# Kernel tuning notes

Measured on AMD Instinct MI355X. Metric: run time of the kernel, lower is better.

Reference implementation:

```python
import jax, jax.numpy as jnp
import numpy as np

CHANNELS = 256
BATCH, H, W = 32, 56, 56
K = 26  # round(256 * 0.1)
BOOST_STRENGTH = 1.0


def setup_inputs() -> dict:
    key = jax.random.key(0)
    k1, k2 = jax.random.split(key)
    x = jax.random.normal(k1, (BATCH, CHANNELS, H, W), dtype=jnp.float32)
    duty_cycle = jax.random.uniform(k2, (1, CHANNELS, 1, 1), dtype=jnp.float32)
    return {"x": x, "duty_cycle": duty_cycle, "k": K,
            "boost_strength": jnp.float32(BOOST_STRENGTH)}


def reference(x, duty_cycle, k, boost_strength):
    # boost_activations: x.detach() * exp(-boost_strength * duty_cycle)
    # (boost_strength > 0 in this configuration)
    boosted = jax.lax.stop_gradient(x) * jnp.exp(-boost_strength * duty_cycle)
    # local kwinners: per (b,h,w) location, kthvalue over channels at index
    # C - k + 1 (1-based ascending) == k-th largest boosted value.
    C = x.shape[1]
    sorted_b = jnp.sort(boosted, axis=1)           # ascending over channels
    threshold = sorted_b[:, C - k:C - k + 1, :, :]  # [B,1,H,W], k-th largest
    # off_mask = boosted < threshold; masked_fill with 0 keeps boosted >= threshold
    keep = boosted >= threshold
    return jnp.where(keep, x, jnp.zeros((), dtype=x.dtype))
```

## Files before the change

### kernel.cpp

```cpp
#include <hip/hip_runtime.h>
#include <math.h>

#define C_CH 256
#define KTOP 26
#define HWSZ 3136
#define NPIX 100352
#define CHW  (C_CH * HWSZ)
#define PIX_PER_BLK 32
#define BLKS_PER_IMG 98
#define CPT 32

typedef float f32x4 __attribute__((ext_vector_type(4)));

__device__ __forceinline__ void ce_desc(float& a, float& b) {
    float mx = fmaxf(a, b); float mn = fminf(a, b); a = mx; b = mn;
}
__device__ __forceinline__ void ce_asc(float& a, float& b) {
    float mn = fminf(a, b); float mx = fmaxf(a, b); a = mn; b = mx;
}

__device__ __forceinline__ void sort32_desc(float* v) {
#pragma unroll
    for (int k = 2; k <= 32; k <<= 1) {
#pragma unroll
        for (int j = k >> 1; j > 0; j >>= 1) {
#pragma unroll
            for (int i = 0; i < 32; ++i) {
                int l = i ^ j;
                if (l > i) {
                    if ((i & k) == 0) ce_desc(v[i], v[l]);
                    else              ce_asc(v[i], v[l]);
                }
            }
        }
    }
}

__device__ __forceinline__ void clean32_desc(float* v) {
#pragma unroll
    for (int j = 16; j > 0; j >>= 1) {
#pragma unroll
        for (int i = 0; i < 32; ++i) {
            int l = i ^ j;
            if (l > i) ce_desc(v[i], v[l]);
        }
    }
}

__device__ __forceinline__ void merge26(float* a, const float* __restrict__ src) {
    float h[32];
#pragma unroll
    for (int i = 0; i < 32; ++i) {
        float u = (i < KTOP)      ? a[i]        : -INFINITY;
        float w = (31 - i < KTOP) ? src[31 - i] : -INFINITY;
        h[i] = fmaxf(u, w);
    }
    clean32_desc(h);
#pragma unroll
    for (int j = 0; j < KTOP; ++j) a[j] = h[j];
}

__global__ __launch_bounds__(256, 4) void kwinners_kernel(
    const float* __restrict__ x, const float* __restrict__ duty,
    const float* __restrict__ bsp, float* __restrict__ out)
{
    __shared__ float s[C_CH];
    __shared__ float tile[C_CH][PIX_PER_BLK];
    __shared__ float pub[2][PIX_PER_BLK][26];

    const int t   = threadIdx.x;
    const int w   = t >> 6;
    const int l   = t & 63;
    const int pl  = l & 31;
    const int hf  = l >> 5;
    const int blk = blockIdx.x;
    const int b   = blk / BLKS_PER_IMG;
    const int hw0 = (blk - b * BLKS_PER_IMG) * PIX_PER_BLK;

    {
        const int row0 = w * 64;
        const float* gp = x + (size_t)b * CHW + (size_t)(row0 + (l >> 3)) * HWSZ
                            + hw0 + (l & 7) * 4;
#pragma unroll
        for (int it = 0; it < 8; ++it) {
            __builtin_amdgcn_global_load_lds(
                (const __attribute__((address_space(1))) void*)(gp + (size_t)it * 8 * HWSZ),
                (__attribute__((address_space(3))) void*)&tile[row0 + it * 8][0],
                16, 0, 0);
        }
    }

    {
        float bs = bsp[0];
        float m = -(bs * duty[t]);
        s[t] = (float)exp((double)m);
    }
    __syncthreads();

    const int c0 = w * 64 + hf * 32;
    const float* sc = s + c0;

    float v[CPT];
#pragma unroll
    for (int i = 0; i < CPT; ++i) v[i] = tile[c0 + i][pl] * sc[i];

    sort32_desc(v);

    float a[KTOP];
    {
        float h[32];
#pragma unroll
        for (int i = 0; i < 32; ++i) {
            float u  = (i < KTOP)      ? v[i] : -INFINITY;
            float pw = (31 - i < KTOP) ? __shfl_xor(v[31 - i], 32) : -INFINITY;
            h[i] = fmaxf(u, pw);
        }
        clean32_desc(h);
#pragma unroll
        for (int j = 0; j < KTOP; ++j) a[j] = h[j];
    }

    if ((w & 1) && l < 32) {
        float* dst = pub[w >> 1][pl];
#pragma unroll
        for (int j = 0; j < KTOP; ++j) dst[j] = a[j];
    }
    __syncthreads();

    if (w == 0) {
        merge26(a, pub[0][pl]);
    } else if (w == 2) {
        merge26(a, pub[1][pl]);
        if (l < 32) {
            float* dst = pub[1][pl];
#pragma unroll
            for (int j = 0; j < KTOP; ++j) dst[j] = a[j];
        }
    }
    __syncthreads();

    if (w == 0) {
        const float* src = pub[1][pl];
        float h[32];
#pragma unroll
        for (int i = 0; i < 32; ++i) {
            float u  = (i < KTOP)      ? a[i]        : -INFINITY;
            float wv = (31 - i < KTOP) ? src[31 - i] : -INFINITY;
            h[i] = fmaxf(u, wv);
        }
        float l16[16];
#pragma unroll
        for (int i = 0; i < 16; ++i) l16[i] = fminf(h[i], h[i + 16]);
        float l8[8];
#pragma unroll
        for (int i = 0; i < 8; ++i)  l8[i]  = fminf(l16[i], l16[i + 8]);
        float h4[4];
#pragma unroll
        for (int i = 0; i < 4; ++i)  h4[i]  = fmaxf(l8[i], l8[i + 4]);
        float h2[2];
#pragma unroll
        for (int i = 0; i < 2; ++i)  h2[i]  = fmaxf(h4[i], h4[i + 2]);
        if (l < 32) pub[0][pl][0] = fminf(h2[0], h2[1]);
    }
    __syncthreads();

    {
        const int pg   = l & 7;
        const int r8   = l >> 3;
        const int row0 = w * 64;
        const float t0 = pub[0][pg * 4 + 0][0];
        const float t1 = pub[0][pg * 4 + 1][0];
        const float t2 = pub[0][pg * 4 + 2][0];
        const float t3 = pub[0][pg * 4 + 3][0];

        float* opb = out + (size_t)b * CHW + (size_t)(row0 + r8) * HWSZ
                         + hw0 + pg * 4;
#pragma unroll
        for (int it = 0; it < 8; ++it) {
            const int r = row0 + it * 8 + r8;
            const f32x4 xv = *reinterpret_cast<const f32x4*>(&tile[r][pg * 4]);
            const float scv = s[r];
            f32x4 res;
            res.x = (xv.x * scv >= t0) ? xv.x : 0.0f;
            res.y = (xv.y * scv >= t1) ? xv.y : 0.0f;
            res.z = (xv.z * scv >= t2) ? xv.z : 0.0f;
            res.w = (xv.w * scv >= t3) ? xv.w : 0.0f;
            __builtin_nontemporal_store(
                res, reinterpret_cast<f32x4*>(&opb[(size_t)(it * 8) * HWSZ]));
        }
    }
}

extern "C" void kernel_launch(void* const* d_in, const int* in_sizes, int n_in,
                              void* d_out, int out_size, void* d_ws, size_t ws_size,
                              hipStream_t stream) {
    const float* x    = (const float*)d_in[0];
    const float* duty = (const float*)d_in[1];
    const float* bs   = (const float*)d_in[3];
    float* out = (float*)d_out;

    hipLaunchKernelGGL(kwinners_kernel, dim3(NPIX / PIX_PER_BLK), dim3(256), 0,
                       stream, x, duty, bs, out);
}
```

Measured before the change: 38.39 us.

## Reorganize top-k merge into in-wave shuffles with XOR-swizzled LDS tile

Remaps threads so each wave owns 8 pixels, with 8 lanes each sorting 32 channels of a pixel. The cross-wave merge tree through shared memory and its extra barriers is replaced by in-wave shuffle merges (xor 32, 8, 16). The global-to-LDS tile load and the output store use an XOR swizzle on the pixel-quad column, and the scale array is padded, both to avoid LDS bank conflicts under the new column-strided access. All 64 lanes now do sort and merge work instead of waves idling during the reduction, at the cost of more shuffle traffic and more complex indexing.

```diff
diff --git a/kernel.cpp b/kernel.cpp
--- a/kernel.cpp
+++ b/kernel.cpp
@@ -8,7 +8,6 @@
 #define CHW  (C_CH * HWSZ)
 #define PIX_PER_BLK 32
 #define BLKS_PER_IMG 98
-#define CPT 32
 
 typedef float f32x4 __attribute__((ext_vector_type(4)));
 
@@ -47,12 +46,12 @@
     }
 }
 
-__device__ __forceinline__ void merge26(float* a, const float* __restrict__ src) {
+__device__ __forceinline__ void shfl_merge26(float* a, int mask) {
     float h[32];
 #pragma unroll
     for (int i = 0; i < 32; ++i) {
-        float u = (i < KTOP)      ? a[i]        : -INFINITY;
-        float w = (31 - i < KTOP) ? src[31 - i] : -INFINITY;
+        float u = (i < KTOP)      ? a[i] : -INFINITY;
+        float w = (31 - i < KTOP) ? __shfl_xor(a[31 - i], mask) : -INFINITY;
         h[i] = fmaxf(u, w);
     }
     clean32_desc(h);
@@ -64,28 +63,30 @@
     const float* __restrict__ x, const float* __restrict__ duty,
     const float* __restrict__ bsp, float* __restrict__ out)
 {
-    __shared__ float s[C_CH];
+    __shared__ float s[264];
     __shared__ float tile[C_CH][PIX_PER_BLK];
-    __shared__ float pub[2][PIX_PER_BLK][26];
+    __shared__ float thr_s[PIX_PER_BLK];
 
     const int t   = threadIdx.x;
     const int w   = t >> 6;
     const int l   = t & 63;
-    const int pl  = l & 31;
-    const int hf  = l >> 5;
+    const int g   = l >> 3;
+    const int p3  = l & 7;
+    const int px  = w * 8 + p3;
     const int blk = blockIdx.x;
     const int b   = blk / BLKS_PER_IMG;
     const int hw0 = (blk - b * BLKS_PER_IMG) * PIX_PER_BLK;
 
     {
-        const int row0 = w * 64;
-        const float* gp = x + (size_t)b * CHW + (size_t)(row0 + (l >> 3)) * HWSZ
-                            + hw0 + (l & 7) * 4;
 #pragma unroll
         for (int it = 0; it < 8; ++it) {
+            const int row = w * 64 + it * 8 + g;
+            const int lq  = p3 ^ ((row >> 5) & 7);
+            const float* gp = x + (size_t)b * CHW + (size_t)row * HWSZ
+                                + hw0 + lq * 4;
             __builtin_amdgcn_global_load_lds(
-                (const __attribute__((address_space(1))) void*)(gp + (size_t)it * 8 * HWSZ),
-                (__attribute__((address_space(3))) void*)&tile[row0 + it * 8][0],
+                (const __attribute__((address_space(1))) void*)gp,
+                (__attribute__((address_space(3))) void*)&tile[w * 64 + it * 8][0],
                 16, 0, 0);
         }
     }
@@ -93,16 +94,15 @@
     {
         float bs = bsp[0];
         float m = -(bs * duty[t]);
-        s[t] = (float)exp((double)m);
+        s[(t >> 5) * 33 + (t & 31)] = (float)exp((double)m);
     }
     __syncthreads();
 
-    const int c0 = w * 64 + hf * 32;
-    const float* sc = s + c0;
-
-    float v[CPT];
+    const int pcol = px ^ (g << 2);
+    float v[32];
 #pragma unroll
-    for (int i = 0; i < CPT; ++i) v[i] = tile[c0 + i][pl] * sc[i];
+    for (int i = 0; i < 32; ++i)
+        v[i] = tile[g * 32 + i][pcol] * s[g * 33 + i];
 
     sort32_desc(v);
 
@@ -110,43 +110,23 @@
     {
         float h[32];
 #pragma unroll
-        for (int i = 0; i < 32; ++i) {
-            float u  = (i < KTOP)      ? v[i] : -INFINITY;
-            float pw = (31 - i < KTOP) ? __shfl_xor(v[31 - i], 32) : -INFINITY;
-            h[i] = fmaxf(u, pw);
-        }
+        for (int i = 0; i < 32; ++i)
+            h[i] = fmaxf(v[i], __shfl_xor(v[31 - i], 32));
         clean32_desc(h);
 #pragma unroll
         for (int j = 0; j < KTOP; ++j) a[j] = h[j];
     }
 
-    if ((w & 1) && l < 32) {
-        float* dst = pub[w >> 1][pl];
-#pragma unroll
-        for (int j = 0; j < KTOP; ++j) dst[j] = a[j];
-    }
-    __syncthreads();
+    shfl_merge26(a, 8);
 
-    if (w == 0) {
-        merge26(a, pub[0][pl]);
-    } else if (w == 2) {
-        merge26(a, pub[1][pl]);
-        if (l < 32) {
-            float* dst = pub[1][pl];
-#pragma unroll
-            for (int j = 0; j < KTOP; ++j) dst[j] = a[j];
-        }
-    }
-    __syncthreads();
-
-    if (w == 0) {
-        const float* src = pub[1][pl];
+    float thr;
+    {
         float h[32];
 #pragma unroll
         for (int i = 0; i < 32; ++i) {
-            float u  = (i < KTOP)      ? a[i]        : -INFINITY;
-            float wv = (31 - i < KTOP) ? src[31 - i] : -INFINITY;
-            h[i] = fmaxf(u, wv);
+            float u  = (i < KTOP)      ? a[i] : -INFINITY;
+            float pw = (31 - i < KTOP) ? __shfl_xor(a[31 - i], 16) : -INFINITY;
+            h[i] = fmaxf(u, pw);
         }
         float l16[16];
 #pragma unroll
@@ -160,33 +140,32 @@
         float h2[2];
 #pragma unroll
         for (int i = 0; i < 2; ++i)  h2[i]  = fmaxf(h4[i], h4[i + 2]);
-        if (l < 32) pub[0][pl][0] = fminf(h2[0], h2[1]);
+        thr = fminf(h2[0], h2[1]);
     }
+    if (g == 0) thr_s[px] = thr;
     __syncthreads();
 
     {
-        const int pg   = l & 7;
-        const int r8   = l >> 3;
-        const int row0 = w * 64;
-        const float t0 = pub[0][pg * 4 + 0][0];
-        const float t1 = pub[0][pg * 4 + 1][0];
-        const float t2 = pub[0][pg * 4 + 2][0];
-        const float t3 = pub[0][pg * 4 + 3][0];
-
-        float* opb = out + (size_t)b * CHW + (size_t)(row0 + r8) * HWSZ
-                         + hw0 + pg * 4;
+        const int pg = p3;
+        const int r8 = g;
 #pragma unroll
         for (int it = 0; it < 8; ++it) {
-            const int r = row0 + it * 8 + r8;
+            const int r  = w * 64 + it * 8 + r8;
+            const int lq = pg ^ ((r >> 5) & 7);
             const f32x4 xv = *reinterpret_cast<const f32x4*>(&tile[r][pg * 4]);
-            const float scv = s[r];
+            const float scv = s[(r >> 5) * 33 + (r & 31)];
+            const float t0 = thr_s[lq * 4 + 0];
+            const float t1 = thr_s[lq * 4 + 1];
+            const float t2 = thr_s[lq * 4 + 2];
+            const float t3 = thr_s[lq * 4 + 3];
             f32x4 res;
             res.x = (xv.x * scv >= t0) ? xv.x : 0.0f;
             res.y = (xv.y * scv >= t1) ? xv.y : 0.0f;
             res.z = (xv.z * scv >= t2) ? xv.z : 0.0f;
             res.w = (xv.w * scv >= t3) ? xv.w : 0.0f;
             __builtin_nontemporal_store(
-                res, reinterpret_cast<f32x4*>(&opb[(size_t)(it * 8) * HWSZ]));
+                res, reinterpret_cast<f32x4*>(
+                    out + (size_t)b * CHW + (size_t)r * HWSZ + hw0 + lq * 4));
         }
     }
 }
```

Result: slower. 43.22 us (+12.6%).

## Process 64 pixels per 512-thread block with swizzled LDS tile layout

Applied to the files above, without the earlier changes.

Doubles the pixel tile per block to 64 and the block size to 512 threads. Eight waves split into channel quarters and pixel halves, and the merge tree now runs in two parallel chains. The global-to-LDS loads use a rotated column swizzle so each 256-byte row segment can be fetched and later read without bank conflicts. This gives longer contiguous global rows and fewer blocks, at the cost of more LDS per block, which may lower occupancy, and more complex indexing.

```diff
diff --git a/kernel.cpp b/kernel.cpp
--- a/kernel.cpp
+++ b/kernel.cpp
@@ -6,9 +6,8 @@
 #define HWSZ 3136
 #define NPIX 100352
 #define CHW  (C_CH * HWSZ)
-#define PIX_PER_BLK 32
-#define BLKS_PER_IMG 98
-#define CPT 32
+#define PIX_PER_BLK 64
+#define BLKS_PER_IMG 49
 
 typedef float f32x4 __attribute__((ext_vector_type(4)));
 
@@ -60,68 +59,77 @@
     for (int j = 0; j < KTOP; ++j) a[j] = h[j];
 }
 
-__global__ __launch_bounds__(256, 4) void kwinners_kernel(
+__global__ __launch_bounds__(512, 4) void kwinners_kernel(
     const float* __restrict__ x, const float* __restrict__ duty,
     const float* __restrict__ bsp, float* __restrict__ out)
 {
     __shared__ float s[C_CH];
     __shared__ float tile[C_CH][PIX_PER_BLK];
-    __shared__ float pub[2][PIX_PER_BLK][26];
+    __shared__ float pub[4][32][KTOP];
+    __shared__ float thr_s[PIX_PER_BLK];
 
     const int t   = threadIdx.x;
     const int w   = t >> 6;
     const int l   = t & 63;
-    const int pl  = l & 31;
-    const int hf  = l >> 5;
     const int blk = blockIdx.x;
     const int b   = blk / BLKS_PER_IMG;
     const int hw0 = (blk - b * BLKS_PER_IMG) * PIX_PER_BLK;
 
     {
-        const int row0 = w * 64;
-        const float* gp = x + (size_t)b * CHW + (size_t)(row0 + (l >> 3)) * HWSZ
-                            + hw0 + (l & 7) * 4;
+        const int p    = l & 15;
+        const int rsub = l >> 4;
 #pragma unroll
         for (int it = 0; it < 8; ++it) {
+            const int Rb = w * 32 + it * 4;
+            const int R  = Rb + rsub;
+            const int lq = (p - R) & 15;
+            const float* gp = x + (size_t)b * CHW + (size_t)R * HWSZ
+                                + hw0 + lq * 4;
             __builtin_amdgcn_global_load_lds(
-                (const __attribute__((address_space(1))) void*)(gp + (size_t)it * 8 * HWSZ),
-                (__attribute__((address_space(3))) void*)&tile[row0 + it * 8][0],
+                (const __attribute__((address_space(1))) void*)gp,
+                (__attribute__((address_space(3))) void*)&tile[Rb][0],
                 16, 0, 0);
         }
     }
 
-    {
+    if (t < C_CH) {
         float bs = bsp[0];
         float m = -(bs * duty[t]);
         s[t] = (float)exp((double)m);
     }
     __syncthreads();
 
-    const int c0 = w * 64 + hf * 32;
-    const float* sc = s + c0;
-
-    float v[CPT];
-#pragma unroll
-    for (int i = 0; i < CPT; ++i) v[i] = tile[c0 + i][pl] * sc[i];
-
+    const int qc = w >> 1;
+    const int ph = w & 1;
+    const int hf = l >> 5;
+    const int pl = l & 31;
+    const int px = ph * 32 + pl;
+    const int c0 = qc * 64 + hf * 32;
+
+    float v[32];
+    {
+        int col = ((((px >> 2) + c0) & 15) << 2) | (px & 3);
+#pragma unroll
+        for (int i = 0; i < 32; ++i) {
+            v[i] = tile[c0 + i][col] * s[c0 + i];
+            col = (col + 4) & 63;
+        }
+    }
     sort32_desc(v);
 
     float a[KTOP];
     {
         float h[32];
 #pragma unroll
-        for (int i = 0; i < 32; ++i) {
-            float u  = (i < KTOP)      ? v[i] : -INFINITY;
-            float pw = (31 - i < KTOP) ? __shfl_xor(v[31 - i], 32) : -INFINITY;
-            h[i] = fmaxf(u, pw);
-        }
+        for (int i = 0; i < 32; ++i)
+            h[i] = fmaxf(v[i], __shfl_xor(v[31 - i], 32));
         clean32_desc(h);
 #pragma unroll
         for (int j = 0; j < KTOP; ++j) a[j] = h[j];
     }
 
-    if ((w & 1) && l < 32) {
-        float* dst = pub[w >> 1][pl];
+    if ((w == 2 || w == 3 || w == 6 || w == 7) && hf == 0) {
+        float* dst = pub[(w < 4) ? (w - 2) : (w - 4)][pl];
 #pragma unroll
         for (int j = 0; j < KTOP; ++j) dst[j] = a[j];
     }
@@ -129,18 +137,27 @@
 
     if (w == 0) {
         merge26(a, pub[0][pl]);
-    } else if (w == 2) {
+    } else if (w == 1) {
         merge26(a, pub[1][pl]);
-        if (l < 32) {
-            float* dst = pub[1][pl];
+    } else if (w == 4) {
+        merge26(a, pub[2][pl]);
+        if (hf == 0) {
+            float* dst = pub[2][pl];
 #pragma unroll
             for (int j = 0; j < KTOP; ++j) dst[j] = a[j];
         }
-    }
-    __syncthreads();
-
-    if (w == 0) {
-        const float* src = pub[1][pl];
+    } else if (w == 5) {
+        merge26(a, pub[3][pl]);
+        if (hf == 0) {
+            float* dst = pub[3][pl];
+#pragma unroll
+            for (int j = 0; j < KTOP; ++j) dst[j] = a[j];
+        }
+    }
+    __syncthreads();
+
+    if (w <= 1) {
+        const float* src = pub[2 + w][pl];
         float h[32];
 #pragma unroll
         for (int i = 0; i < 32; ++i) {
@@ -160,33 +177,31 @@
         float h2[2];
 #pragma unroll
         for (int i = 0; i < 2; ++i)  h2[i]  = fmaxf(h4[i], h4[i + 2]);
-        if (l < 32) pub[0][pl][0] = fminf(h2[0], h2[1]);
-    }
-    __syncthreads();
-
-    {
-        const int pg   = l & 7;
-        const int r8   = l >> 3;
-        const int row0 = w * 64;
-        const float t0 = pub[0][pg * 4 + 0][0];
-        const float t1 = pub[0][pg * 4 + 1][0];
-        const float t2 = pub[0][pg * 4 + 2][0];
-        const float t3 = pub[0][pg * 4 + 3][0];
-
-        float* opb = out + (size_t)b * CHW + (size_t)(row0 + r8) * HWSZ
-                         + hw0 + pg * 4;
+        if (hf == 0) thr_s[w * 32 + pl] = fminf(h2[0], h2[1]);
+    }
+    __syncthreads();
+
+    {
+        const int pg = l & 15;
+        const int r4 = l >> 4;
+        const float t0 = thr_s[pg * 4 + 0];
+        const float t1 = thr_s[pg * 4 + 1];
+        const float t2 = thr_s[pg * 4 + 2];
+        const float t3 = thr_s[pg * 4 + 3];
 #pragma unroll
         for (int it = 0; it < 8; ++it) {
-            const int r = row0 + it * 8 + r8;
-            const f32x4 xv = *reinterpret_cast<const f32x4*>(&tile[r][pg * 4]);
-            const float scv = s[r];
+            const int row = w * 32 + it * 4 + r4;
+            const int pq  = (pg + row) & 15;
+            const f32x4 xv = *reinterpret_cast<const f32x4*>(&tile[row][pq * 4]);
+            const float scv = s[row];
             f32x4 res;
             res.x = (xv.x * scv >= t0) ? xv.x : 0.0f;
             res.y = (xv.y * scv >= t1) ? xv.y : 0.0f;
             res.z = (xv.z * scv >= t2) ? xv.z : 0.0f;
             res.w = (xv.w * scv >= t3) ? xv.w : 0.0f;
             __builtin_nontemporal_store(
-                res, reinterpret_cast<f32x4*>(&opb[(size_t)(it * 8) * HWSZ]));
+                res, reinterpret_cast<f32x4*>(
+                    out + (size_t)b * CHW + (size_t)row * HWSZ + hw0 + pg * 4));
         }
     }
 }
@@ -199,6 +214,6 @@
     const float* bs   = (const float*)d_in[3];
     float* out = (float*)d_out;
 
-    hipLaunchKernelGGL(kwinners_kernel, dim3(NPIX / PIX_PER_BLK), dim3(256), 0,
+    hipLaunchKernelGGL(kwinners_kernel, dim3(NPIX / PIX_PER_BLK), dim3(512), 0,
                        stream, x, duty, bs, out);
 }
```

Result: slower. 43.85 us (+14.2%).

## Double-buffer two pixel tiles per block to overlap loads with sorting

Applied to the files above, without the earlier changes.

Each block now handles two 32-pixel tiles, using two LDS buffers. The second tile's global-to-LDS load is issued while the first tile is being sorted and written out, so memory latency is hidden behind compute. The grid size is halved and launch bounds drop to 2 blocks per CU. Synchronisation moves to explicit waitcnt and barrier macros. The extra LDS and the lower occupancy may cut latency hiding across blocks, and the second tile's compute is not overlapped with anything.

```diff
diff --git a/kernel.cpp b/kernel.cpp
--- a/kernel.cpp
+++ b/kernel.cpp
@@ -6,11 +6,22 @@
 #define HWSZ 3136
 #define NPIX 100352
 #define CHW  (C_CH * HWSZ)
-#define PIX_PER_BLK 32
-#define BLKS_PER_IMG 98
-#define CPT 32
+#define PPB  32
+#define TPI  98
+#define CPT  32
 
 typedef float f32x4 __attribute__((ext_vector_type(4)));
+
+#define BAR_LDS() do { \
+    asm volatile("s_waitcnt lgkmcnt(0)" ::: "memory"); \
+    __builtin_amdgcn_sched_barrier(0); \
+    __builtin_amdgcn_s_barrier(); \
+} while (0)
+
+#define WAIT_VM() do { \
+    asm volatile("s_waitcnt vmcnt(0)" ::: "memory"); \
+    __builtin_amdgcn_sched_barrier(0); \
+} while (0)
 
 __device__ __forceinline__ void ce_desc(float& a, float& b) {
     float mx = fmaxf(a, b); float mn = fminf(a, b); a = mx; b = mn;
@@ -60,27 +71,36 @@
     for (int j = 0; j < KTOP; ++j) a[j] = h[j];
 }
 
-__global__ __launch_bounds__(256, 4) void kwinners_kernel(
+__global__ __launch_bounds__(256, 2) void kwinners_kernel(
     const float* __restrict__ x, const float* __restrict__ duty,
     const float* __restrict__ bsp, float* __restrict__ out)
 {
     __shared__ float s[C_CH];
-    __shared__ float tile[C_CH][PIX_PER_BLK];
-    __shared__ float pub[2][PIX_PER_BLK][26];
-
-    const int t   = threadIdx.x;
-    const int w   = t >> 6;
-    const int l   = t & 63;
-    const int pl  = l & 31;
-    const int hf  = l >> 5;
-    const int blk = blockIdx.x;
-    const int b   = blk / BLKS_PER_IMG;
-    const int hw0 = (blk - b * BLKS_PER_IMG) * PIX_PER_BLK;
-
-    {
+    __shared__ float tileA[C_CH][PPB];
+    __shared__ float tileB[C_CH][PPB];
+    __shared__ float pub[2][PPB][26];
+
+    const int t  = threadIdx.x;
+    const int w  = t >> 6;
+    const int l  = t & 63;
+    const int pl = l & 31;
+    const int hf = l >> 5;
+
+    const int tid0 = blockIdx.x * 2;
+    const int b0   = tid0 / TPI;
+    const int h0   = (tid0 - b0 * TPI) * PPB;
+    const int tid1 = tid0 + 1;
+    const int b1   = tid1 / TPI;
+    const int h1   = (tid1 - b1 * TPI) * PPB;
+
+    const float* xb0 = x + (size_t)b0 * CHW + h0;
+    const float* xb1 = x + (size_t)b1 * CHW + h1;
+    float* ob0 = out + (size_t)b0 * CHW + h0;
+    float* ob1 = out + (size_t)b1 * CHW + h1;
+
+    auto stage = [&](float (*tile)[PPB], const float* xb) {
         const int row0 = w * 64;
-        const float* gp = x + (size_t)b * CHW + (size_t)(row0 + (l >> 3)) * HWSZ
-                            + hw0 + (l & 7) * 4;
+        const float* gp = xb + (size_t)(row0 + (l >> 3)) * HWSZ + (l & 7) * 4;
 #pragma unroll
         for (int it = 0; it < 8; ++it) {
             __builtin_amdgcn_global_load_lds(
@@ -88,107 +108,119 @@
                 (__attribute__((address_space(3))) void*)&tile[row0 + it * 8][0],
                 16, 0, 0);
         }
-    }
-
+    };
+
+    auto process = [&](float (*tile)[PPB], const float* xn, float (*tn)[PPB],
+                       float* ob) {
+        BAR_LDS();
+
+        const int c0 = w * 64 + hf * 32;
+        const float* sc = s + c0;
+
+        float v[CPT];
+#pragma unroll
+        for (int i = 0; i < CPT; ++i) v[i] = tile[c0 + i][pl] * sc[i];
+
+        if (xn) stage(tn, xn);
+
+        sort32_desc(v);
+
+        float a[KTOP];
+        {
+            float h[32];
+#pragma unroll
+            for (int i = 0; i < 32; ++i) {
+                float u  = (i < KTOP)      ? v[i] : -INFINITY;
+                float pw = (31 - i < KTOP) ? __shfl_xor(v[31 - i], 32) : -INFINITY;
+                h[i] = fmaxf(u, pw);
+            }
+            clean32_desc(h);
+#pragma unroll
+            for (int j = 0; j < KTOP; ++j) a[j] = h[j];
+        }
+
+        if ((w & 1) && l < 32) {
+            float* dst = pub[w >> 1][pl];
+#pragma unroll
+            for (int j = 0; j < KTOP; ++j) dst[j] = a[j];
+        }
+        BAR_LDS();
+
+        if (w == 0) {
+            merge26(a, pub[0][pl]);
+        } else if (w == 2) {
+            merge26(a, pub[1][pl]);
+            if (l < 32) {
+                float* dst = pub[1][pl];
+#pragma unroll
+                for (int j = 0; j < KTOP; ++j) dst[j] = a[j];
+            }
+        }
+        BAR_LDS();
+
+        if (w == 0) {
+            const float* src = pub[1][pl];
+            float h[32];
+#pragma unroll
+            for (int i = 0; i < 32; ++i) {
+                float u  = (i < KTOP)      ? a[i]        : -INFINITY;
+                float wv = (31 - i < KTOP) ? src[31 - i] : -INFINITY;
+                h[i] = fmaxf(u, wv);
+            }
+            float l16[16];
+#pragma unroll
+            for (int i = 0; i < 16; ++i) l16[i] = fminf(h[i], h[i + 16]);
+            float l8[8];
+#pragma unroll
+            for (int i = 0; i < 8; ++i)  l8[i]  = fminf(l16[i], l16[i + 8]);
+            float h4[4];
+#pragma unroll
+            for (int i = 0; i < 4; ++i)  h4[i]  = fmaxf(l8[i], l8[i + 4]);
+            float h2[2];
+#pragma unroll
+            for (int i = 0; i < 2; ++i)  h2[i]  = fmaxf(h4[i], h4[i + 2]);
+            if (l < 32) pub[0][pl][0] = fminf(h2[0], h2[1]);
+        }
+        BAR_LDS();
+
+        {
+            const int pg   = l & 7;
+            const int r8   = l >> 3;
+            const int row0 = w * 64;
+            const float t0 = pub[0][pg * 4 + 0][0];
+            const float t1 = pub[0][pg * 4 + 1][0];
+            const float t2 = pub[0][pg * 4 + 2][0];
+            const float t3 = pub[0][pg * 4 + 3][0];
+
+            float* opb = ob + (size_t)(row0 + r8) * HWSZ + pg * 4;
+#pragma unroll
+            for (int it = 0; it < 8; ++it) {
+                const int r = row0 + it * 8 + r8;
+                const f32x4 xv = *reinterpret_cast<const f32x4*>(&tile[r][pg * 4]);
+                const float scv = s[r];
+                f32x4 res;
+                res.x = (xv.x * scv >= t0) ? xv.x : 0.0f;
+                res.y = (xv.y * scv >= t1) ? xv.y : 0.0f;
+                res.z = (xv.z * scv >= t2) ? xv.z : 0.0f;
+                res.w = (xv.w * scv >= t3) ? xv.w : 0.0f;
+                __builtin_nontemporal_store(
+                    res, reinterpret_cast<f32x4*>(&opb[(size_t)(it * 8) * HWSZ]));
+            }
+        }
+    };
+
+    stage(tileA, xb0);
     {
         float bs = bsp[0];
         float m = -(bs * duty[t]);
         s[t] = (float)exp((double)m);
     }
-    __syncthreads();
-
-    const int c0 = w * 64 + hf * 32;
-    const float* sc = s + c0;
-
-    float v[CPT];
-#pragma unroll
-    for (int i = 0; i < CPT; ++i) v[i] = tile[c0 + i][pl] * sc[i];
-
-    sort32_desc(v);
-
-    float a[KTOP];
-    {
-        float h[32];
-#pragma unroll
-        for (int i = 0; i < 32; ++i) {
-            float u  = (i < KTOP)      ? v[i] : -INFINITY;
-            float pw = (31 - i < KTOP) ? __shfl_xor(v[31 - i], 32) : -INFINITY;
-            h[i] = fmaxf(u, pw);
-        }
-        clean32_desc(h);
-#pragma unroll
-        for (int j = 0; j < KTOP; ++j) a[j] = h[j];
-    }
-
-    if ((w & 1) && l < 32) {
-        float* dst = pub[w >> 1][pl];
-#pragma unroll
-        for (int j = 0; j < KTOP; ++j) dst[j] = a[j];
-    }
-    __syncthreads();
-
-    if (w == 0) {
-        merge26(a, pub[0][pl]);
-    } else if (w == 2) {
-        merge26(a, pub[1][pl]);
-        if (l < 32) {
-            float* dst = pub[1][pl];
-#pragma unroll
-            for (int j = 0; j < KTOP; ++j) dst[j] = a[j];
-        }
-    }
-    __syncthreads();
-
-    if (w == 0) {
-        const float* src = pub[1][pl];
-        float h[32];
-#pragma unroll
-        for (int i = 0; i < 32; ++i) {
-            float u  = (i < KTOP)      ? a[i]        : -INFINITY;
-            float wv = (31 - i < KTOP) ? src[31 - i] : -INFINITY;
-            h[i] = fmaxf(u, wv);
-        }
-        float l16[16];
-#pragma unroll
-        for (int i = 0; i < 16; ++i) l16[i] = fminf(h[i], h[i + 16]);
-        float l8[8];
-#pragma unroll
-        for (int i = 0; i < 8; ++i)  l8[i]  = fminf(l16[i], l16[i + 8]);
-        float h4[4];
-#pragma unroll
-        for (int i = 0; i < 4; ++i)  h4[i]  = fmaxf(l8[i], l8[i + 4]);
-        float h2[2];
-#pragma unroll
-        for (int i = 0; i < 2; ++i)  h2[i]  = fmaxf(h4[i], h4[i + 2]);
-        if (l < 32) pub[0][pl][0] = fminf(h2[0], h2[1]);
-    }
-    __syncthreads();
-
-    {
-        const int pg   = l & 7;
-        const int r8   = l >> 3;
-        const int row0 = w * 64;
-        const float t0 = pub[0][pg * 4 + 0][0];
-        const float t1 = pub[0][pg * 4 + 1][0];
-        const float t2 = pub[0][pg * 4 + 2][0];
-        const float t3 = pub[0][pg * 4 + 3][0];
-
-        float* opb = out + (size_t)b * CHW + (size_t)(row0 + r8) * HWSZ
-                         + hw0 + pg * 4;
-#pragma unroll
-        for (int it = 0; it < 8; ++it) {
-            const int r = row0 + it * 8 + r8;
-            const f32x4 xv = *reinterpret_cast<const f32x4*>(&tile[r][pg * 4]);
-            const float scv = s[r];
-            f32x4 res;
-            res.x = (xv.x * scv >= t0) ? xv.x : 0.0f;
-            res.y = (xv.y * scv >= t1) ? xv.y : 0.0f;
-            res.z = (xv.z * scv >= t2) ? xv.z : 0.0f;
-            res.w = (xv.w * scv >= t3) ? xv.w : 0.0f;
-            __builtin_nontemporal_store(
-                res, reinterpret_cast<f32x4*>(&opb[(size_t)(it * 8) * HWSZ]));
-        }
-    }
+
+    WAIT_VM();
+    process(tileA, xb1, tileB, ob0);
+
+    WAIT_VM();
+    process(tileB, nullptr, nullptr, ob1);
 }
 
 extern "C" void kernel_launch(void* const* d_in, const int* in_sizes, int n_in,
@@ -199,6 +231,6 @@
     const float* bs   = (const float*)d_in[3];
     float* out = (float*)d_out;
 
-    hipLaunchKernelGGL(kwinners_kernel, dim3(NPIX / PIX_PER_BLK), dim3(256), 0,
+    hipLaunchKernelGGL(kwinners_kernel, dim3(NPIX / (PPB * 2)), dim3(256), 0,
                        stream, x, duty, bs, out);
 }
```

Result: slower. 47.47 us (+23.6%).
